# Performance work log

Measured on AMD Instinct MI355X. Metric: run time of the kernel, lower is better.

Reference implementation:

```python
import jax, jax.numpy as jnp
import numpy as np

SEQ, BATCH, D_IN, HIDDEN = 2048, 64, 512, 512


def setup_inputs() -> dict:
    key = jax.random.key(0)
    k_x, k_wi, k_wh = jax.random.split(key, 3)
    scale_in = 1.0 / np.sqrt(D_IN)      # ~lecun_normal fan_in
    scale_h = 1.0 / np.sqrt(HIDDEN)
    return {
        "x": jax.random.normal(k_x, (SEQ, BATCH, D_IN), dtype=jnp.float32),
        "c0": jnp.zeros((BATCH, HIDDEN), dtype=jnp.float32),
        "h0": jnp.zeros((BATCH, HIDDEN), dtype=jnp.float32),
        "Wi": jax.random.normal(k_wi, (D_IN, 4 * HIDDEN), dtype=jnp.float32) * scale_in,
        "Wh": jax.random.normal(k_wh, (HIDDEN, 4 * HIDDEN), dtype=jnp.float32) * scale_h,
        "b": jnp.zeros((4 * HIDDEN,), dtype=jnp.float32),
    }


def reference(x, c0, h0, Wi, Wh, b):
    # flax LSTMCell scanned over the leading (time) axis.
    # Gate order: i, f, g, o. Input projection has no bias in flax;
    # hidden projection carries the bias -> combined into single b.
    def step(carry, xt):
        c, h = carry
        z = xt @ Wi + h @ Wh + b            # [B, 4H]
        i, f, g, o = jnp.split(z, 4, axis=-1)
        i = jax.nn.sigmoid(i)
        f = jax.nn.sigmoid(f)
        g = jnp.tanh(g)
        o = jax.nn.sigmoid(o)
        c_new = f * c + i * g
        h_new = o * jnp.tanh(c_new)
        return (c_new, h_new), h_new

    (cT, hT), ys = jax.lax.scan(step, (c0, h0), x)
    return cT, hT, ys  # final carry + stacked hidden states [S, B, H]
```

## Files before the change

### kernel.cpp

```cpp
#include <hip/hip_runtime.h>

#define SEQ    2048
#define BATCH  64
#define DIN    512
#define HID    512
#define GATES  2048
#define NBLK   256
#define NT     256
#define TC     8
#define ZST    65

typedef short bf16v8 __attribute__((ext_vector_type(8)));
typedef float f32x4  __attribute__((ext_vector_type(4)));

static __device__ __forceinline__ unsigned short f2bfbits(float f) {
    union { __bf16 h; unsigned short s; } u;
    u.h = (__bf16)f;
    return u.s;
}

static __device__ __forceinline__ bf16v8 cvt8(const float* __restrict__ p) {
    float4 a = *(const float4*)(p);
    float4 b = *(const float4*)(p + 4);
    union { __bf16 h[8]; bf16v8 v; } u;
    u.h[0] = (__bf16)a.x; u.h[1] = (__bf16)a.y;
    u.h[2] = (__bf16)a.z; u.h[3] = (__bf16)a.w;
    u.h[4] = (__bf16)b.x; u.h[5] = (__bf16)b.y;
    u.h[6] = (__bf16)b.z; u.h[7] = (__bf16)b.w;
    return u.v;
}

static __device__ __forceinline__ float sigm(float v) {
    return 1.0f / (1.0f + __expf(-v));
}
static __device__ __forceinline__ float ftanh(float v) {
    return 1.0f - 2.0f / (__expf(2.0f * v) + 1.0f);
}

__global__ void __launch_bounds__(NT, 1) lstm_v12(
    const float* __restrict__ x,  const float* __restrict__ c0,
    const float* __restrict__ h0, const float* __restrict__ Wi,
    const float* __restrict__ Wh, const float* __restrict__ bias,
    float* __restrict__ out, unsigned int* flags, unsigned int* mall,
    unsigned int* claim, unsigned short* hglob)
{
    __shared__ unsigned short wi_lds[64 * 512];
    __shared__ unsigned short wh_lds[64 * 512];
    __shared__ float zxb[64 * ZST];
    __shared__ unsigned short h_lds[8 * 512];
    __shared__ float ys_lds[TC * 8 * 16];
    __shared__ int xs_lds[2];
    __shared__ int abortf;

    const int tid  = threadIdx.x;
    const int lane = tid & 63;
    const int wv   = tid >> 6;
    const int col  = lane & 15;
    const int rgrp = lane >> 4;
    const int c7   = col & 7;
    const int c3   = col & 3;

    unsigned int zu = 0; asm volatile("" : "+v"(zu));

    unsigned int xcd;
    asm volatile("s_getreg_b32 %0, hwreg(HW_REG_XCC_ID)" : "=s"(xcd));
    if (tid == 0) {
        abortf = 0;
        unsigned int slot = __hip_atomic_fetch_add(&claim[(xcd & 7) * 16], 1u,
                               __ATOMIC_RELAXED, __HIP_MEMORY_SCOPE_AGENT);
        xs_lds[0] = (int)(xcd & 7);
        xs_lds[1] = (int)(slot & 31);
    }
    __syncthreads();
    const int x_ = xs_lds[0];
    const int s_ = xs_lds[1];

    for (int idx = tid; idx < 64 * 512; idx += NT) {
        const int lc = idx & 63, k = idx >> 6;
        const int c = lc & 15, w = lc >> 4;
        const int gc = (c >> 2) * HID + s_ * 16 + w * 4 + (c & 3);
        const int sidx = lc * 512 + ((((k >> 3) ^ (c & 7)) << 3) | (k & 7));
        wi_lds[sidx] = f2bfbits(Wi[(size_t)k * GATES + gc]);
        wh_lds[sidx] = f2bfbits(Wh[(size_t)k * GATES + gc]);
    }

    if (tid == 0)
        (void)__hip_atomic_exchange(&flags[(x_ * 32 + s_) * 16], 0u,
                                    __ATOMIC_RELAXED,
                                    __HIP_MEMORY_SCOPE_WORKGROUP);

    if (tid < 128) {
        const int row = tid >> 4, j = tid & 15;
        hglob[(x_ * 8 + row) * 512 + s_ * 16 + j] =
            f2bfbits(h0[(8 * x_ + row) * HID + s_ * 16 + j]);
    }
    asm volatile("s_waitcnt vmcnt(0)" ::: "memory");
    __syncthreads();

    if (tid == 0)
        __hip_atomic_store(&mall[(x_ * 32 + s_) * 16], 1u,
                           __ATOMIC_RELAXED, __HIP_MEMORY_SCOPE_AGENT);
    if (wv == 0) {
        int guard = 0;
        unsigned int v;
        do {
            v = __hip_atomic_load(&mall[(x_ * 32 + (lane & 31)) * 16],
                                  __ATOMIC_RELAXED, __HIP_MEMORY_SCOPE_AGENT);
            if (__all(v >= 1u)) break;
            __builtin_amdgcn_s_sleep(8);
        } while (++guard < (1 << 20));
        if (guard >= (1 << 20)) abortf = 1;
    }
    __syncthreads();
    if (tid == 0) {
        (void)__hip_atomic_exchange(&flags[(x_ * 32 + s_) * 16], 1u,
                                    __ATOMIC_RELAXED,
                                    __HIP_MEMORY_SCOPE_WORKGROUP);
        asm volatile("s_waitcnt vmcnt(0)" ::: "memory");
    }

    bf16v8 whf[16];
    #pragma unroll
    for (int ks = 0; ks < 16; ++ks)
        whf[ks] = *(const bf16v8*)(wh_lds + (wv * 16 + col) * 512 +
                                   (((ks * 4 + rgrp) ^ c7) << 3));

    float bvA[4];
    #pragma unroll
    for (int g = 0; g < 4; ++g)
        bvA[g] = bias[(col >> 2) * HID + s_ * 16 + g * 4 + c3];

    const int hcol = s_ * 16 + 4 * wv + col;
    const bool act = (col < 4) && (rgrp < 2);
    float cv[4];
    #pragma unroll
    for (int r = 0; r < 4; ++r)
        cv[r] = act ? c0[(8 * x_ + rgrp * 4 + r) * HID + hcol] : 0.0f;

    for (int t0 = 0; t0 < SEQ; t0 += TC) {
        if (t0 > 0) {
            const int ft = tid >> 5, fr = (tid >> 2) & 7, fc = (tid & 3) * 4;
            const float4 v = *(const float4*)(ys_lds + (ft * 8 + fr) * 16 + fc);
            *(float4*)(out + 2 * (size_t)BATCH * HID +
                       ((size_t)(t0 - TC + ft) * BATCH + 8 * x_ + fr) * HID +
                       s_ * 16 + fc) = v;
        }

        {
            f32x4 za0 = {0,0,0,0}, za1 = {0,0,0,0}, za2 = {0,0,0,0}, za3 = {0,0,0,0};
            const int rr = wv * 16 + col;
            const float* xrow = x + ((size_t)(t0 + (rr >> 3)) * BATCH +
                                     8 * x_ + (rr & 7)) * DIN;
            #pragma unroll
            for (int ks = 0; ks < 16; ++ks) {
                const bf16v8 axv = cvt8(xrow + ks * 32 + rgrp * 8);
                const int gsw = ((ks * 4 + rgrp) ^ c7) << 3;
                const bf16v8 b0 = *(const bf16v8*)(wi_lds + (col) * 512 + gsw);
                const bf16v8 b1 = *(const bf16v8*)(wi_lds + (16 + col) * 512 + gsw);
                const bf16v8 b2 = *(const bf16v8*)(wi_lds + (32 + col) * 512 + gsw);
                const bf16v8 b3 = *(const bf16v8*)(wi_lds + (48 + col) * 512 + gsw);
                za0 = __builtin_amdgcn_mfma_f32_16x16x32_bf16(axv, b0, za0, 0, 0, 0);
                za1 = __builtin_amdgcn_mfma_f32_16x16x32_bf16(axv, b1, za1, 0, 0, 0);
                za2 = __builtin_amdgcn_mfma_f32_16x16x32_bf16(axv, b2, za2, 0, 0, 0);
                za3 = __builtin_amdgcn_mfma_f32_16x16x32_bf16(axv, b3, za3, 0, 0, 0);
            }
            #pragma unroll
            for (int r = 0; r < 4; ++r) {
                const int zr = (wv * 16 + rgrp * 4 + r) * ZST;
                zxb[zr + col]      = za0[r] + bvA[0];
                zxb[zr + 16 + col] = za1[r] + bvA[1];
                zxb[zr + 32 + col] = za2[r] + bvA[2];
                zxb[zr + 48 + col] = za3[r] + bvA[3];
            }
        }
        __syncthreads();

        for (int tt = 0; tt < TC; ++tt) {
            const int t = t0 + tt;

            if (wv == 0 && !abortf) {
                const unsigned int tgt = (unsigned int)t + 1u;
                unsigned int* fp = &flags[(x_ * 32 + (lane & 31)) * 16];
                int guard = 0;
                while (true) {
                    unsigned int v = 0xffffffffu;
                    if (lane < 32)
                        v = __hip_atomic_fetch_add(fp, zu, __ATOMIC_RELAXED,
                                                   __HIP_MEMORY_SCOPE_WORKGROUP);
                    if (__all(v >= tgt)) break;
                    if (++guard > (1 << 22)) { abortf = 1; break; }
                }
            }
            __syncthreads();

            {
                __builtin_amdgcn_fence(__ATOMIC_ACQUIRE, "agent");
                const int row = tid >> 5, ks2 = (tid >> 1) & 15, rg0 = (tid & 1) * 2;
                const unsigned long long* src = (const unsigned long long*)
                    (hglob + (((t & 1) * 8 + x_) * 8 + row) * 512)
                    + (ks2 * 8 + rg0 * 2);
                const unsigned long long q0 = src[0];
                const unsigned long long q1 = src[1];
                const unsigned long long q2 = src[2];
                const unsigned long long q3 = src[3];
                const int base = row * 512 + ks2 * 32;
                unsigned long long* d0 = (unsigned long long*)
                    (h_lds + base + ((rg0 ^ (row & 3)) << 3));
                d0[0] = q0; d0[1] = q1;
                unsigned long long* d1 = (unsigned long long*)
                    (h_lds + base + (((rg0 + 1) ^ (row & 3)) << 3));
                d1[0] = q2; d1[1] = q3;
            }
            __syncthreads();

            f32x4 accA, accB = {0, 0, 0, 0};
            {
                const int zr = (tt * 8 + (rgrp & 1) * 4) * ZST + wv * 16 + col;
                accA[0] = zxb[zr];           accA[1] = zxb[zr + ZST];
                accA[2] = zxb[zr + 2 * ZST]; accA[3] = zxb[zr + 3 * ZST];
            }
            const int abase = (col & 7) * 512 + ((rgrp ^ c3) << 3);
            #pragma unroll
            for (int ks = 0; ks < 16; ks += 2) {
                const bf16v8 a0 = *(const bf16v8*)(h_lds + abase + ks * 32);
                const bf16v8 a1 = *(const bf16v8*)(h_lds + abase + ks * 32 + 32);
                accA = __builtin_amdgcn_mfma_f32_16x16x32_bf16(a0, whf[ks],     accA, 0, 0, 0);
                accB = __builtin_amdgcn_mfma_f32_16x16x32_bf16(a1, whf[ks + 1], accB, 0, 0, 0);
            }

            float z[4], zf[4], zg[4], zo[4];
            #pragma unroll
            for (int r = 0; r < 4; ++r) z[r] = accA[r] + accB[r];
            #pragma unroll
            for (int r = 0; r < 4; ++r) {
                zf[r] = __shfl_xor(z[r], 4);
                zg[r] = __shfl_xor(z[r], 8);
                zo[r] = __shfl_xor(z[r], 12);
            }

            if (act) {
                #pragma unroll
                for (int r = 0; r < 4; ++r) {
                    const float ig = sigm(z[r]);
                    const float fg = sigm(zf[r]);
                    const float gg = ftanh(zg[r]);
                    const float og = sigm(zo[r]);
                    const float cn = fg * cv[r] + ig * gg;
                    cv[r] = cn;
                    const float hn = og * ftanh(cn);
                    const int row = rgrp * 4 + r;
                    hglob[((((t + 1) & 1) * 8 + x_) * 8 + row) * 512 + hcol] =
                        f2bfbits(hn);
                    ys_lds[(tt * 8 + row) * 16 + 4 * wv + col] = hn;
                    if (t == SEQ - 1) {
                        out[(size_t)(8 * x_ + row) * HID + hcol] = cn;
                        out[(size_t)BATCH * HID + (size_t)(8 * x_ + row) * HID + hcol] = hn;
                    }
                }
            }
            asm volatile("s_waitcnt vmcnt(0)" ::: "memory");
            __syncthreads();
            if (tid == 0) {
                (void)__hip_atomic_exchange(&flags[(x_ * 32 + s_) * 16],
                                            (unsigned int)t + 2u,
                                            __ATOMIC_RELAXED,
                                            __HIP_MEMORY_SCOPE_WORKGROUP);
                asm volatile("s_waitcnt vmcnt(0)" ::: "memory");
            }
        }
    }

    __syncthreads();
    {
        const int ft = tid >> 5, fr = (tid >> 2) & 7, fc = (tid & 3) * 4;
        const float4 v = *(const float4*)(ys_lds + (ft * 8 + fr) * 16 + fc);
        *(float4*)(out + 2 * (size_t)BATCH * HID +
                   ((size_t)(SEQ - TC + ft) * BATCH + 8 * x_ + fr) * HID +
                   s_ * 16 + fc) = v;
    }
}

extern "C" void kernel_launch(void* const* d_in, const int* in_sizes, int n_in,
                              void* d_out, int out_size, void* d_ws, size_t ws_size,
                              hipStream_t stream) {
    const float* x  = (const float*)d_in[0];
    const float* c0 = (const float*)d_in[1];
    const float* h0 = (const float*)d_in[2];
    const float* Wi = (const float*)d_in[3];
    const float* Wh = (const float*)d_in[4];
    const float* b  = (const float*)d_in[5];
    float* out = (float*)d_out;

    char* wsb = (char*)d_ws;
    unsigned int* flags   = (unsigned int*)wsb;
    unsigned int* mall    = (unsigned int*)(wsb + 16384);
    unsigned int* claim   = (unsigned int*)(wsb + 32768);
    unsigned short* hglob = (unsigned short*)(wsb + 36864);

    (void)hipMemsetAsync(wsb, 0, 33280, stream);

    void* args[] = { (void*)&x, (void*)&c0, (void*)&h0, (void*)&Wi,
                     (void*)&Wh, (void*)&b, (void*)&out, (void*)&flags,
                     (void*)&mall, (void*)&claim, (void*)&hglob };
    (void)hipLaunchCooperativeKernel((void*)lstm_v12, dim3(NBLK), dim3(NT),
                                     args, 0, stream);
}
```

Measured before the change: 22.22 ms.

## Remove block barriers: per-wave polling, h staging and LDS-counter flag release

Drops all per-timestep __syncthreads: every wave now polls the cross-block flags itself, stages its own copy of h into LDS, and an LDS atomic counter lets the last-arriving wave publish the block's step flag. The Wi input projection is restructured so each wave computes its own gate column for all rows, removing the barrier before zxb use. The block doubles to 512 threads, with the extra four waves spinning on dummy FMAs until done, apparently to hold the CU clock up or keep the SIMDs busy. Risks include redundant global polling and h loads per wave, and possible LDS races since waves write the shared h_lds/zxb buffers without barriers.

```diff
diff --git a/kernel.cpp b/kernel.cpp
--- a/kernel.cpp
+++ b/kernel.cpp
@@ -6,7 +6,7 @@
 #define HID    512
 #define GATES  2048
 #define NBLK   256
-#define NT     256
+#define NT     512
 #define TC     8
 #define ZST    65
 
@@ -37,7 +37,7 @@
     return 1.0f - 2.0f / (__expf(2.0f * v) + 1.0f);
 }
 
-__global__ void __launch_bounds__(NT, 1) lstm_v12(
+__global__ void __launch_bounds__(NT, 1) lstm_v16(
     const float* __restrict__ x,  const float* __restrict__ c0,
     const float* __restrict__ h0, const float* __restrict__ Wi,
     const float* __restrict__ Wh, const float* __restrict__ bias,
@@ -51,6 +51,8 @@
     __shared__ float ys_lds[TC * 8 * 16];
     __shared__ int xs_lds[2];
     __shared__ int abortf;
+    __shared__ int done_lds;
+    __shared__ unsigned int cnt_lds;
 
     const int tid  = threadIdx.x;
     const int lane = tid & 63;
@@ -65,7 +67,7 @@
     unsigned int xcd;
     asm volatile("s_getreg_b32 %0, hwreg(HW_REG_XCC_ID)" : "=s"(xcd));
     if (tid == 0) {
-        abortf = 0;
+        abortf = 0; done_lds = 0; cnt_lds = 0u;
         unsigned int slot = __hip_atomic_fetch_add(&claim[(xcd & 7) * 16], 1u,
                                __ATOMIC_RELAXED, __HIP_MEMORY_SCOPE_AGENT);
         xs_lds[0] = (int)(xcd & 7);
@@ -119,17 +121,32 @@
         asm volatile("s_waitcnt vmcnt(0)" ::: "memory");
     }
 
+    if (wv >= 4) {
+        float b0 = 1.0f + (float)lane * 1e-6f, b1 = b0 + 0.1f,
+              b2 = b0 + 0.2f, b3 = b0 + 0.3f;
+        int guard = 0;
+        while (__hip_atomic_load(&done_lds, __ATOMIC_RELAXED,
+                                 __HIP_MEMORY_SCOPE_WORKGROUP) == 0
+               && ++guard < (1 << 24)) {
+            #pragma unroll
+            for (int i = 0; i < 64; ++i) {
+                b0 = __builtin_fmaf(b0, 1.0000001f, 1e-9f);
+                b1 = __builtin_fmaf(b1, 1.0000001f, 1e-9f);
+                b2 = __builtin_fmaf(b2, 1.0000001f, 1e-9f);
+                b3 = __builtin_fmaf(b3, 1.0000001f, 1e-9f);
+            }
+            asm volatile("" : "+v"(b0), "+v"(b1), "+v"(b2), "+v"(b3));
+        }
+        return;
+    }
+
     bf16v8 whf[16];
     #pragma unroll
     for (int ks = 0; ks < 16; ++ks)
         whf[ks] = *(const bf16v8*)(wh_lds + (wv * 16 + col) * 512 +
                                    (((ks * 4 + rgrp) ^ c7) << 3));
 
-    float bvA[4];
-    #pragma unroll
-    for (int g = 0; g < 4; ++g)
-        bvA[g] = bias[(col >> 2) * HID + s_ * 16 + g * 4 + c3];
-
+    const float bv = bias[(col >> 2) * HID + s_ * 16 + wv * 4 + c3];
     const int hcol = s_ * 16 + 4 * wv + col;
     const bool act = (col < 4) && (rgrp < 2);
     float cv[4];
@@ -139,46 +156,35 @@
 
     for (int t0 = 0; t0 < SEQ; t0 += TC) {
         if (t0 > 0) {
-            const int ft = tid >> 5, fr = (tid >> 2) & 7, fc = (tid & 3) * 4;
-            const float4 v = *(const float4*)(ys_lds + (ft * 8 + fr) * 16 + fc);
+            const int ft = lane >> 3, fr = lane & 7;
+            const float4 v = *(const float4*)(ys_lds + (ft * 8 + fr) * 16 + 4 * wv);
             *(float4*)(out + 2 * (size_t)BATCH * HID +
                        ((size_t)(t0 - TC + ft) * BATCH + 8 * x_ + fr) * HID +
-                       s_ * 16 + fc) = v;
+                       s_ * 16 + 4 * wv) = v;
         }
 
-        {
-            f32x4 za0 = {0,0,0,0}, za1 = {0,0,0,0}, za2 = {0,0,0,0}, za3 = {0,0,0,0};
-            const int rr = wv * 16 + col;
+        #pragma unroll
+        for (int m = 0; m < 4; ++m) {
+            const int rr = m * 16 + col;
             const float* xrow = x + ((size_t)(t0 + (rr >> 3)) * BATCH +
                                      8 * x_ + (rr & 7)) * DIN;
+            f32x4 za = {0.f, 0.f, 0.f, 0.f};
             #pragma unroll
             for (int ks = 0; ks < 16; ++ks) {
                 const bf16v8 axv = cvt8(xrow + ks * 32 + rgrp * 8);
                 const int gsw = ((ks * 4 + rgrp) ^ c7) << 3;
-                const bf16v8 b0 = *(const bf16v8*)(wi_lds + (col) * 512 + gsw);
-                const bf16v8 b1 = *(const bf16v8*)(wi_lds + (16 + col) * 512 + gsw);
-                const bf16v8 b2 = *(const bf16v8*)(wi_lds + (32 + col) * 512 + gsw);
-                const bf16v8 b3 = *(const bf16v8*)(wi_lds + (48 + col) * 512 + gsw);
-                za0 = __builtin_amdgcn_mfma_f32_16x16x32_bf16(axv, b0, za0, 0, 0, 0);
-                za1 = __builtin_amdgcn_mfma_f32_16x16x32_bf16(axv, b1, za1, 0, 0, 0);
-                za2 = __builtin_amdgcn_mfma_f32_16x16x32_bf16(axv, b2, za2, 0, 0, 0);
-                za3 = __builtin_amdgcn_mfma_f32_16x16x32_bf16(axv, b3, za3, 0, 0, 0);
-            }
-            #pragma unroll
-            for (int r = 0; r < 4; ++r) {
-                const int zr = (wv * 16 + rgrp * 4 + r) * ZST;
-                zxb[zr + col]      = za0[r] + bvA[0];
-                zxb[zr + 16 + col] = za1[r] + bvA[1];
-                zxb[zr + 32 + col] = za2[r] + bvA[2];
-                zxb[zr + 48 + col] = za3[r] + bvA[3];
-            }
+                const bf16v8 b0 = *(const bf16v8*)(wi_lds + (wv * 16 + col) * 512 + gsw);
+                za = __builtin_amdgcn_mfma_f32_16x16x32_bf16(axv, b0, za, 0, 0, 0);
+            }
+            #pragma unroll
+            for (int r = 0; r < 4; ++r)
+                zxb[(m * 16 + rgrp * 4 + r) * ZST + wv * 16 + col] = za[r] + bv;
         }
-        __syncthreads();
 
         for (int tt = 0; tt < TC; ++tt) {
             const int t = t0 + tt;
 
-            if (wv == 0 && !abortf) {
+            if (!abortf) {
                 const unsigned int tgt = (unsigned int)t + 1u;
                 unsigned int* fp = &flags[(x_ * 32 + (lane & 31)) * 16];
                 int guard = 0;
@@ -191,27 +197,27 @@
                     if (++guard > (1 << 22)) { abortf = 1; break; }
                 }
             }
-            __syncthreads();
 
             {
                 __builtin_amdgcn_fence(__ATOMIC_ACQUIRE, "agent");
-                const int row = tid >> 5, ks2 = (tid >> 1) & 15, rg0 = (tid & 1) * 2;
-                const unsigned long long* src = (const unsigned long long*)
-                    (hglob + (((t & 1) * 8 + x_) * 8 + row) * 512)
-                    + (ks2 * 8 + rg0 * 2);
-                const unsigned long long q0 = src[0];
-                const unsigned long long q1 = src[1];
-                const unsigned long long q2 = src[2];
-                const unsigned long long q3 = src[3];
-                const int base = row * 512 + ks2 * 32;
-                unsigned long long* d0 = (unsigned long long*)
-                    (h_lds + base + ((rg0 ^ (row & 3)) << 3));
-                d0[0] = q0; d0[1] = q1;
-                unsigned long long* d1 = (unsigned long long*)
-                    (h_lds + base + (((rg0 + 1) ^ (row & 3)) << 3));
-                d1[0] = q2; d1[1] = q3;
-            }
-            __syncthreads();
+                const int row8 = lane >> 3, seg = lane & 7;
+                const unsigned long long* sp = (const unsigned long long*)
+                    (hglob + (((t & 1) * 8 + x_) * 8 + row8) * 512);
+                #pragma unroll
+                for (int j = 0; j < 2; ++j) {
+                    const int ks2 = seg * 2 + j;
+                    #pragma unroll
+                    for (int rg = 0; rg < 4; ++rg) {
+                        const int kofs = ks2 * 32 + rg * 8;
+                        const unsigned long long q0 = sp[kofs >> 2];
+                        const unsigned long long q1 = sp[(kofs >> 2) + 1];
+                        unsigned long long* dp = (unsigned long long*)
+                            (h_lds + row8 * 512 + ks2 * 32 +
+                             ((rg ^ (row8 & 3)) << 3));
+                        dp[0] = q0; dp[1] = q1;
+                    }
+                }
+            }
 
             f32x4 accA, accB = {0, 0, 0, 0};
             {
@@ -258,26 +264,32 @@
                     }
                 }
             }
+
             asm volatile("s_waitcnt vmcnt(0)" ::: "memory");
-            __syncthreads();
-            if (tid == 0) {
-                (void)__hip_atomic_exchange(&flags[(x_ * 32 + s_) * 16],
-                                            (unsigned int)t + 2u,
-                                            __ATOMIC_RELAXED,
-                                            __HIP_MEMORY_SCOPE_WORKGROUP);
-                asm volatile("s_waitcnt vmcnt(0)" ::: "memory");
+            if (lane == 0) {
+                const unsigned int old = __hip_atomic_fetch_add(&cnt_lds, 1u,
+                        __ATOMIC_ACQ_REL, __HIP_MEMORY_SCOPE_WORKGROUP);
+                if (old == 4u * (unsigned int)t + 3u) {
+                    (void)__hip_atomic_exchange(&flags[(x_ * 32 + s_) * 16],
+                                                (unsigned int)t + 2u,
+                                                __ATOMIC_RELAXED,
+                                                __HIP_MEMORY_SCOPE_WORKGROUP);
+                    asm volatile("s_waitcnt vmcnt(0)" ::: "memory");
+                }
             }
         }
     }
 
-    __syncthreads();
     {
-        const int ft = tid >> 5, fr = (tid >> 2) & 7, fc = (tid & 3) * 4;
-        const float4 v = *(const float4*)(ys_lds + (ft * 8 + fr) * 16 + fc);
+        const int ft = lane >> 3, fr = lane & 7;
+        const float4 v = *(const float4*)(ys_lds + (ft * 8 + fr) * 16 + 4 * wv);
         *(float4*)(out + 2 * (size_t)BATCH * HID +
                    ((size_t)(SEQ - TC + ft) * BATCH + 8 * x_ + fr) * HID +
-                   s_ * 16 + fc) = v;
-    }
+                   s_ * 16 + 4 * wv) = v;
+    }
+    if (wv == 0 && lane == 0)
+        __hip_atomic_store(&done_lds, 1, __ATOMIC_RELAXED,
+                           __HIP_MEMORY_SCOPE_WORKGROUP);
 }
 
 extern "C" void kernel_launch(void* const* d_in, const int* in_sizes, int n_in,
@@ -302,6 +314,6 @@
     void* args[] = { (void*)&x, (void*)&c0, (void*)&h0, (void*)&Wi,
                      (void*)&Wh, (void*)&b, (void*)&out, (void*)&flags,
                      (void*)&mall, (void*)&claim, (void*)&hglob };
-    (void)hipLaunchCooperativeKernel((void*)lstm_v12, dim3(NBLK), dim3(NT),
+    (void)hipLaunchCooperativeKernel((void*)lstm_v16, dim3(NBLK), dim3(NT),
                                      args, 0, stream);
 }
```

Measured after the change: 41.48 ms. +86.7%, slower.
